# Kernel tuning notes

Hardware: AMD Instinct MI355X
Metric: run time of the kernel (lower is better)

The kernel has to match this reference:

```python
import jax, jax.numpy as jnp
import numpy as np


def setup_inputs() -> dict:
    key = jax.random.key(0)
    k1, k2, k3, k4 = jax.random.split(key, 4)
    N, E, F, H = 100000, 3200000, 128, 128
    x = jax.random.normal(k1, (N, F), dtype=jnp.float32)
    edge_index = jax.random.randint(k2, (2, E), 0, N, dtype=jnp.int64)
    # GCNConv learned params (glorot-like weight, zero-ish bias init replaced by small random)
    W = jax.random.normal(k3, (F, H), dtype=jnp.float32) * (1.0 / np.sqrt(F))
    b = jax.random.normal(k4, (H,), dtype=jnp.float32) * 0.01
    return {"x": x, "edge_index": edge_index, "W": W, "b": b}


def reference(x, edge_index, W, b):
    # PyG GCNConv: add self-loops, symmetric degree normalization,
    # linear transform, gather-scale-scatter aggregation, bias.
    N = x.shape[0]
    loop = jnp.arange(N, dtype=edge_index.dtype)
    src = jnp.concatenate([edge_index[0], loop])  # [E+N]
    dst = jnp.concatenate([edge_index[1], loop])  # [E+N]
    # degree of destination nodes (edge_weight = 1)
    deg = jax.ops.segment_sum(jnp.ones_like(dst, dtype=x.dtype), dst, num_segments=N)
    dinv = jnp.where(deg > 0, jax.lax.rsqrt(deg), 0.0)
    norm = dinv[src] * dinv[dst]  # [E+N]
    h = x @ W  # [N, H]
    msgs = norm[:, None] * h[src]  # gather + scale, [E+N, H]
    out = jax.ops.segment_sum(msgs, dst, num_segments=N)  # scatter-add
    return out + b
```

## Files before the change

kernel.cpp:

```cpp
#include <hip/hip_runtime.h>

#define FEAT 128
#define BSH 7
#define BNODES 128
#define ATILE 4096
#define MAXNB 1024
#define STILE 1024

typedef __attribute__((ext_vector_type(8))) short bf16x8;
typedef __attribute__((ext_vector_type(4))) float f32x4;

__global__ void k_zero_i32(int* __restrict__ p, int n) {
    int i = blockIdx.x * blockDim.x + threadIdx.x;
    if (i < n) p[i] = 0;
}

__global__ void k_count(const int* __restrict__ dst, int* __restrict__ cnt, int E) {
    int i = blockIdx.x * blockDim.x + threadIdx.x;
    if (i < E) atomicAdd(&cnt[dst[i]], 1);
}

__global__ void k_dinv(const int* __restrict__ cnt, float* __restrict__ dinv, int N) {
    int i = blockIdx.x * blockDim.x + threadIdx.x;
    if (i < N) dinv[i] = rsqrtf((float)cnt[i] + 1.0f);
}

__global__ void k_bucket_base(const int* __restrict__ offs, int* __restrict__ cur, int NB) {
    int b = blockIdx.x * blockDim.x + threadIdx.x;
    if (b < NB) cur[b] = offs[b << BSH];
}

__device__ inline unsigned int f2bf(float f) {
    unsigned int u = __float_as_uint(f);
    return (u + 0x7FFFu + ((u >> 16) & 1u)) >> 16;
}

__global__ void k_cvt_bf16(const float* __restrict__ x, unsigned int* __restrict__ xbf,
                           long long n8) {
    long long i = (long long)blockIdx.x * blockDim.x + threadIdx.x;
    if (i >= n8) return;
    float4 a = ((const float4*)x)[i * 2];
    float4 c = ((const float4*)x)[i * 2 + 1];
    uint4 o;
    o.x = f2bf(a.x) | (f2bf(a.y) << 16);
    o.y = f2bf(a.z) | (f2bf(a.w) << 16);
    o.z = f2bf(c.x) | (f2bf(c.y) << 16);
    o.w = f2bf(c.z) | (f2bf(c.w) << 16);
    ((uint4*)xbf)[i] = o;
}

__global__ void k_cvt_w(const float* __restrict__ W, unsigned short* __restrict__ wt) {
    int i = blockIdx.x * blockDim.x + threadIdx.x;
    if (i >= FEAT * FEAT) return;
    int n = i >> 7, k = i & 127;
    wt[i] = (unsigned short)f2bf(W[k * FEAT + n]);
}

__global__ __launch_bounds__(256) void k_hist_bucket(const int* __restrict__ dst,
                                                     int* __restrict__ bCnt, int E, int NB) {
    __shared__ int h[MAXNB];
    int tid = threadIdx.x;
    for (int i = tid; i < NB; i += 256) h[i] = 0;
    __syncthreads();
    int base = blockIdx.x * ATILE;
    int end = min(base + ATILE, E);
    for (int e = base + tid; e < end; e += 256)
        atomicAdd(&h[dst[e] >> BSH], 1);
    __syncthreads();
    for (int i = tid; i < NB; i += 256)
        if (h[i]) atomicAdd(&bCnt[i], h[i]);
}

__global__ void k_scan_bucket(const int* __restrict__ bCnt, int* __restrict__ bOffs,
                              int* __restrict__ cur, int NB, int E) {
    __shared__ int s[256];
    int t = threadIdx.x;
    int carry = 0;
    for (int base = 0; base < NB; base += 256) {
        int i = base + t;
        int v = (i < NB) ? bCnt[i] : 0;
        s[t] = v; __syncthreads();
        for (int o = 1; o < 256; o <<= 1) {
            int add = (t >= o) ? s[t - o] : 0;
            __syncthreads();
            s[t] += add;
            __syncthreads();
        }
        if (i < NB) { int ex = s[t] - v + carry; bOffs[i] = ex; cur[i] = ex; }
        __syncthreads();
        carry += s[255];
        __syncthreads();
    }
    if (t == 0) bOffs[NB] = E;
}

__global__ void k_scan_partial(const int* __restrict__ cnt, int* __restrict__ part, int N) {
    __shared__ int s[256];
    int base = blockIdx.x * STILE;
    int t = threadIdx.x;
    int sum = 0;
#pragma unroll
    for (int k = 0; k < 4; ++k) {
        int i = base + t * 4 + k;
        if (i < N) sum += cnt[i];
    }
    s[t] = sum; __syncthreads();
    for (int off = 128; off > 0; off >>= 1) {
        if (t < off) s[t] += s[t + off];
        __syncthreads();
    }
    if (t == 0) part[blockIdx.x] = s[0];
}

__global__ void k_scan_top(int* __restrict__ part, int nTiles) {
    __shared__ int s[256];
    int t = threadIdx.x;
    int carry = 0;
    for (int base = 0; base < nTiles; base += 256) {
        int i = base + t;
        int v = (i < nTiles) ? part[i] : 0;
        s[t] = v; __syncthreads();
        for (int o = 1; o < 256; o <<= 1) {
            int add = (t >= o) ? s[t - o] : 0;
            __syncthreads();
            s[t] += add;
            __syncthreads();
        }
        if (i < nTiles) part[i] = (s[t] - v) + carry;
        __syncthreads();
        carry += s[255];
        __syncthreads();
    }
}

__global__ void k_scan_final(const int* __restrict__ cnt, const int* __restrict__ part,
                             int* __restrict__ offs, int N) {
    __shared__ int s[256];
    int base = blockIdx.x * STILE;
    int t = threadIdx.x;
    int v[4]; int sum = 0;
#pragma unroll
    for (int k = 0; k < 4; ++k) {
        int i = base + t * 4 + k;
        v[k] = (i < N) ? cnt[i] : 0;
        sum += v[k];
    }
    s[t] = sum; __syncthreads();
    for (int o = 1; o < 256; o <<= 1) {
        int add = (t >= o) ? s[t - o] : 0;
        __syncthreads();
        s[t] += add;
        __syncthreads();
    }
    int excl = (s[t] - sum) + part[blockIdx.x];
#pragma unroll
    for (int k = 0; k < 4; ++k) {
        int i = base + t * 4 + k;
        if (i < N) offs[i] = excl;
        excl += v[k];
    }
}

__global__ __launch_bounds__(256) void k_bin(const int* __restrict__ src,
                                             const int* __restrict__ dst,
                                             int* __restrict__ cur,
                                             unsigned int* __restrict__ pairs,
                                             int E, int NB) {
    __shared__ int hist[MAXNB];
    __shared__ int tbase[MAXNB];
    __shared__ int sc[256];
    __shared__ unsigned int stM[ATILE];
    __shared__ unsigned short stB[ATILE];

    int tid = threadIdx.x;
    int tileBase = blockIdx.x * ATILE;
    int tileCnt = min(ATILE, E - tileBase);

    for (int i = tid; i < NB; i += 256) hist[i] = 0;
    __syncthreads();

    unsigned int pk[16]; unsigned short bk[16]; unsigned short rk[16];
#pragma unroll
    for (int k = 0; k < 16; ++k) {
        int e = tileBase + k * 256 + tid;
        if (e < E) {
            int s = src[e], d = dst[e];
            int b = d >> BSH;
            int r = atomicAdd(&hist[b], 1);
            pk[k] = (unsigned int)s | ((unsigned int)(d & (BNODES - 1)) << 24);
            bk[k] = (unsigned short)b;
            rk[k] = (unsigned short)r;
        }
    }
    __syncthreads();

    int per = (NB + 255) / 256;
    int myBase = tid * per;
    int partial = 0;
    for (int i = 0; i < per; ++i) {
        int idx = myBase + i;
        if (idx < NB) partial += hist[idx];
    }
    sc[tid] = partial;
    __syncthreads();
    for (int o = 1; o < 256; o <<= 1) {
        int add = (tid >= o) ? sc[tid - o] : 0;
        __syncthreads();
        sc[tid] += add;
        __syncthreads();
    }
    int run = (tid == 0) ? 0 : sc[tid - 1];
    for (int i = 0; i < per; ++i) {
        int idx = myBase + i;
        if (idx < NB) {
            int c = hist[idx];
            hist[idx] = run;
            if (c > 0) {
                int g = atomicAdd(&cur[idx], c);
                tbase[idx] = g - run;
            }
            run += c;
        }
    }
    __syncthreads();

#pragma unroll
    for (int k = 0; k < 16; ++k) {
        int e = tileBase + k * 256 + tid;
        if (e < E) {
            int slot = hist[bk[k]] + (int)rk[k];
            stM[slot] = pk[k];
            stB[slot] = bk[k];
        }
    }
    __syncthreads();

    for (int s = tid; s < tileCnt; s += 256) {
        int gpos = tbase[stB[s]] + s;
        pairs[gpos] = stM[s];
    }
}

__global__ __launch_bounds__(256) void k_fill_local2(const unsigned int* __restrict__ pairs,
                                                     const int* __restrict__ bOffs,
                                                     unsigned int* __restrict__ csr,
                                                     int* __restrict__ g_cnt,
                                                     int* __restrict__ g_offs,
                                                     float* __restrict__ g_dinv,
                                                     int N) {
    __shared__ int lcnt[BNODES];
    __shared__ int lexcl[BNODES];
    __shared__ int lcur[BNODES];
    int b = blockIdx.x;
    int node0 = b << BSH;
    int nn = min(BNODES, N - node0);
    int tid = threadIdx.x;
    int bstart = bOffs[b], bend = bOffs[b + 1];

    if (tid < BNODES) lcnt[tid] = 0;
    __syncthreads();
    for (int i = bstart + tid; i < bend; i += 256)
        atomicAdd(&lcnt[pairs[i] >> 24], 1);
    __syncthreads();
    if (tid < BNODES) lexcl[tid] = lcnt[tid];
    __syncthreads();
    for (int o = 1; o < BNODES; o <<= 1) {
        int add = (tid < BNODES && tid >= o) ? lexcl[tid - o] : 0;
        __syncthreads();
        if (tid < BNODES) lexcl[tid] += add;
        __syncthreads();
    }
    if (tid < BNODES) {
        int ex = bstart + lexcl[tid] - lcnt[tid];
        lcur[tid] = ex;
        if (tid < nn) {
            g_cnt[node0 + tid] = lcnt[tid];
            g_offs[node0 + tid] = ex;
            g_dinv[node0 + tid] = rsqrtf((float)lcnt[tid] + 1.0f);
        }
    }
    __syncthreads();
    for (int i = bstart + tid; i < bend; i += 256) {
        unsigned int p = pairs[i];
        int dl = (int)(p >> 24);
        int pos = atomicAdd(&lcur[dl], 1);
        csr[pos] = p & 0xFFFFFFu;
    }
}

__global__ __launch_bounds__(256) void k_fill_local(const unsigned int* __restrict__ pairs,
                                                    const int* __restrict__ offs,
                                                    unsigned int* __restrict__ csr,
                                                    int N, int E) {
    __shared__ int lcur[BNODES];
    int b = blockIdx.x;
    int node0 = b << BSH;
    int nn = min(BNODES, N - node0);
    int tid = threadIdx.x;
    for (int i = tid; i < nn; i += 256) lcur[i] = offs[node0 + i];
    __syncthreads();
    int start = offs[node0];
    int end = (node0 + BNODES >= N) ? E : offs[node0 + BNODES];
    for (int i = start + tid; i < end; i += 256) {
        unsigned int p = pairs[i];
        int dl = (int)(p >> 24);
        int pos = atomicAdd(&lcur[dl], 1);
        csr[pos] = p & 0xFFFFFFu;
    }
}

__global__ __launch_bounds__(256) void k_aggregate_bf2(const unsigned int* __restrict__ xbf,
                                                       const float* __restrict__ dinv,
                                                       const int* __restrict__ offs,
                                                       const int* __restrict__ cnt,
                                                       const unsigned int* __restrict__ csr,
                                                       unsigned int* __restrict__ aggbf,
                                                       int N) {
    int wid = (blockIdx.x * blockDim.x + threadIdx.x) >> 6;
    int lane = threadIdx.x & 63;
    if (wid >= N) return;
    int n = __builtin_amdgcn_readfirstlane(wid);

    float di = dinv[n];
    int start = offs[n];
    int m = cnt[n];

    unsigned int wself = xbf[(size_t)n * 64 + lane];
    float sl = di * di;
    float2 acc = make_float2(sl * __uint_as_float(wself << 16),
                             sl * __uint_as_float(wself & 0xFFFF0000u));

    int i = 0;
    for (; i + 8 <= m; i += 8) {
        int s[8]; float nr[8]; unsigned int w[8];
#pragma unroll
        for (int u = 0; u < 8; ++u) s[u] = (int)csr[start + i + u];
#pragma unroll
        for (int u = 0; u < 8; ++u) w[u] = xbf[(size_t)s[u] * 64 + lane];
#pragma unroll
        for (int u = 0; u < 8; ++u) nr[u] = dinv[s[u]] * di;
#pragma unroll
        for (int u = 0; u < 8; ++u) {
            acc.x += nr[u] * __uint_as_float(w[u] << 16);
            acc.y += nr[u] * __uint_as_float(w[u] & 0xFFFF0000u);
        }
    }
    for (; i + 4 <= m; i += 4) {
        int s0 = (int)csr[start + i];
        int s1 = (int)csr[start + i + 1];
        int s2 = (int)csr[start + i + 2];
        int s3 = (int)csr[start + i + 3];
        float n0 = dinv[s0] * di, n1 = dinv[s1] * di, n2 = dinv[s2] * di, n3 = dinv[s3] * di;
        unsigned int w0 = xbf[(size_t)s0 * 64 + lane];
        unsigned int w1 = xbf[(size_t)s1 * 64 + lane];
        unsigned int w2 = xbf[(size_t)s2 * 64 + lane];
        unsigned int w3 = xbf[(size_t)s3 * 64 + lane];
        acc.x += n0 * __uint_as_float(w0 << 16);
        acc.y += n0 * __uint_as_float(w0 & 0xFFFF0000u);
        acc.x += n1 * __uint_as_float(w1 << 16);
        acc.y += n1 * __uint_as_float(w1 & 0xFFFF0000u);
        acc.x += n2 * __uint_as_float(w2 << 16);
        acc.y += n2 * __uint_as_float(w2 & 0xFFFF0000u);
        acc.x += n3 * __uint_as_float(w3 << 16);
        acc.y += n3 * __uint_as_float(w3 & 0xFFFF0000u);
    }
    for (; i < m; ++i) {
        int s0 = (int)csr[start + i];
        float n0 = dinv[s0] * di;
        unsigned int w0 = xbf[(size_t)s0 * 64 + lane];
        acc.x += n0 * __uint_as_float(w0 << 16);
        acc.y += n0 * __uint_as_float(w0 & 0xFFFF0000u);
    }
    aggbf[(size_t)n * 64 + lane] = f2bf(acc.x) | (f2bf(acc.y) << 16);
}

__global__ __launch_bounds__(256) void k_aggregate_bf(const float* __restrict__ x,
                                                      const unsigned int* __restrict__ xbf,
                                                      const float* __restrict__ dinv,
                                                      const int* __restrict__ offs,
                                                      const int* __restrict__ cnt,
                                                      const unsigned int* __restrict__ csr,
                                                      float* __restrict__ out, int N) {
    int wid = (blockIdx.x * blockDim.x + threadIdx.x) >> 6;
    int lane = threadIdx.x & 63;
    if (wid >= N) return;
    int n = __builtin_amdgcn_readfirstlane(wid);

    float di = dinv[n];
    int start = offs[n];
    int m = cnt[n];

    float2 a = ((const float2*)(x + (size_t)n * FEAT))[lane];
    float sl = di * di;
    float2 acc = make_float2(a.x * sl, a.y * sl);

    int i = 0;
    for (; i + 4 <= m; i += 4) {
        int s0 = (int)csr[start + i];
        int s1 = (int)csr[start + i + 1];
        int s2 = (int)csr[start + i + 2];
        int s3 = (int)csr[start + i + 3];
        float n0 = dinv[s0] * di, n1 = dinv[s1] * di, n2 = dinv[s2] * di, n3 = dinv[s3] * di;
        unsigned int w0 = xbf[(size_t)s0 * 64 + lane];
        unsigned int w1 = xbf[(size_t)s1 * 64 + lane];
        unsigned int w2 = xbf[(size_t)s2 * 64 + lane];
        unsigned int w3 = xbf[(size_t)s3 * 64 + lane];
        acc.x += n0 * __uint_as_float(w0 << 16);
        acc.y += n0 * __uint_as_float(w0 & 0xFFFF0000u);
        acc.x += n1 * __uint_as_float(w1 << 16);
        acc.y += n1 * __uint_as_float(w1 & 0xFFFF0000u);
        acc.x += n2 * __uint_as_float(w2 << 16);
        acc.y += n2 * __uint_as_float(w2 & 0xFFFF0000u);
        acc.x += n3 * __uint_as_float(w3 << 16);
        acc.y += n3 * __uint_as_float(w3 & 0xFFFF0000u);
    }
    for (; i < m; ++i) {
        int s0 = (int)csr[start + i];
        float n0 = dinv[s0] * di;
        unsigned int w0 = xbf[(size_t)s0 * 64 + lane];
        acc.x += n0 * __uint_as_float(w0 << 16);
        acc.y += n0 * __uint_as_float(w0 & 0xFFFF0000u);
    }
    ((float2*)(out + (size_t)n * FEAT))[lane] = acc;
}

__global__ __launch_bounds__(256) void k_aggregate(const float* __restrict__ x,
                                                   const float* __restrict__ dinv,
                                                   const int* __restrict__ offs,
                                                   const int* __restrict__ cnt,
                                                   const unsigned int* __restrict__ csr,
                                                   float* __restrict__ out, int N) {
    int wid = (blockIdx.x * blockDim.x + threadIdx.x) >> 6;
    int lane = threadIdx.x & 63;
    if (wid >= N) return;
    int n = __builtin_amdgcn_readfirstlane(wid);

    float di = dinv[n];
    int start = offs[n];
    int m = cnt[n];

    float2 a = ((const float2*)(x + (size_t)n * FEAT))[lane];
    float sl = di * di;
    float2 acc = make_float2(a.x * sl, a.y * sl);

    int i = 0;
    for (; i + 4 <= m; i += 4) {
        int s0 = (int)csr[start + i];
        int s1 = (int)csr[start + i + 1];
        int s2 = (int)csr[start + i + 2];
        int s3 = (int)csr[start + i + 3];
        float n0 = dinv[s0] * di, n1 = dinv[s1] * di, n2 = dinv[s2] * di, n3 = dinv[s3] * di;
        float2 v0 = ((const float2*)(x + (size_t)s0 * FEAT))[lane];
        float2 v1 = ((const float2*)(x + (size_t)s1 * FEAT))[lane];
        float2 v2 = ((const float2*)(x + (size_t)s2 * FEAT))[lane];
        float2 v3 = ((const float2*)(x + (size_t)s3 * FEAT))[lane];
        acc.x += n0 * v0.x; acc.y += n0 * v0.y;
        acc.x += n1 * v1.x; acc.y += n1 * v1.y;
        acc.x += n2 * v2.x; acc.y += n2 * v2.y;
        acc.x += n3 * v3.x; acc.y += n3 * v3.y;
    }
    for (; i < m; ++i) {
        int s0 = (int)csr[start + i];
        float n0 = dinv[s0] * di;
        float2 v0 = ((const float2*)(x + (size_t)s0 * FEAT))[lane];
        acc.x += n0 * v0.x; acc.y += n0 * v0.y;
    }
    ((float2*)(out + (size_t)n * FEAT))[lane] = acc;
}

__global__ __launch_bounds__(256) void k_gemm_mfma2(const unsigned short* __restrict__ abf,
                                                    const unsigned short* __restrict__ wt,
                                                    const float* __restrict__ bias,
                                                    float* __restrict__ out, int N) {
    int tid = threadIdx.x;
    int wave = tid >> 6, l = tid & 63;
    int lm = l & 15, lg = l >> 4;
    int rowA = blockIdx.x * 128 + wave * 32;

    f32x4 acc[2][8];
#pragma unroll
    for (int mt = 0; mt < 2; ++mt)
#pragma unroll
        for (int nt = 0; nt < 8; ++nt)
            acc[mt][nt] = (f32x4){0.f, 0.f, 0.f, 0.f};

#pragma unroll
    for (int kk = 0; kk < 4; ++kk) {
        int k = kk * 32 + lg * 8;
        bf16x8 afr[2];
#pragma unroll
        for (int mt = 0; mt < 2; ++mt) {
            int r = rowA + mt * 16 + lm;
            if (r < N)
                afr[mt] = *(const bf16x8*)(abf + (size_t)r * FEAT + k);
            else
                afr[mt] = (bf16x8){0, 0, 0, 0, 0, 0, 0, 0};
        }
#pragma unroll
        for (int nt = 0; nt < 8; ++nt) {
            int col = nt * 16 + lm;
            bf16x8 bfr = *(const bf16x8*)(wt + (size_t)col * FEAT + k);
            acc[0][nt] = __builtin_amdgcn_mfma_f32_16x16x32_bf16(afr[0], bfr, acc[0][nt], 0, 0, 0);
            acc[1][nt] = __builtin_amdgcn_mfma_f32_16x16x32_bf16(afr[1], bfr, acc[1][nt], 0, 0, 0);
        }
    }

#pragma unroll
    for (int nt = 0; nt < 8; ++nt) {
        int col = nt * 16 + lm;
        float bv = bias[col];
#pragma unroll
        for (int mt = 0; mt < 2; ++mt) {
#pragma unroll
            for (int r = 0; r < 4; ++r) {
                int row = rowA + mt * 16 + lg * 4 + r;
                if (row < N) out[(size_t)row * FEAT + col] = acc[mt][nt][r] + bv;
            }
        }
    }
}

__global__ __launch_bounds__(256) void k_gemm_mfma(float* __restrict__ out,
                                                   const unsigned short* __restrict__ wt,
                                                   const float* __restrict__ b, int N) {
    int tid = threadIdx.x;
    int wave = tid >> 6, l = tid & 63;
    int lm = l & 15, lg = l >> 4;
    int rowA = blockIdx.x * 128 + wave * 32;

    f32x4 acc[2][8];
#pragma unroll
    for (int mt = 0; mt < 2; ++mt)
#pragma unroll
        for (int nt = 0; nt < 8; ++nt)
            acc[mt][nt] = (f32x4){0.f, 0.f, 0.f, 0.f};

#pragma unroll
    for (int kk = 0; kk < 4; ++kk) {
        int k = kk * 32 + lg * 8;
        bf16x8 afr[2];
#pragma unroll
        for (int mt = 0; mt < 2; ++mt) {
            int r = rowA + mt * 16 + lm;
            float4 f0 = make_float4(0.f, 0.f, 0.f, 0.f);
            float4 f1 = make_float4(0.f, 0.f, 0.f, 0.f);
            if (r < N) {
                const float* p = out + (size_t)r * FEAT + k;
                f0 = *(const float4*)p;
                f1 = *(const float4*)(p + 4);
            }
            afr[mt][0] = (short)f2bf(f0.x);
            afr[mt][1] = (short)f2bf(f0.y);
            afr[mt][2] = (short)f2bf(f0.z);
            afr[mt][3] = (short)f2bf(f0.w);
            afr[mt][4] = (short)f2bf(f1.x);
            afr[mt][5] = (short)f2bf(f1.y);
            afr[mt][6] = (short)f2bf(f1.z);
            afr[mt][7] = (short)f2bf(f1.w);
        }
#pragma unroll
        for (int nt = 0; nt < 8; ++nt) {
            int col = nt * 16 + lm;
            bf16x8 bfr = *(const bf16x8*)(wt + (size_t)col * FEAT + k);
            acc[0][nt] = __builtin_amdgcn_mfma_f32_16x16x32_bf16(afr[0], bfr, acc[0][nt], 0, 0, 0);
            acc[1][nt] = __builtin_amdgcn_mfma_f32_16x16x32_bf16(afr[1], bfr, acc[1][nt], 0, 0, 0);
        }
    }

#pragma unroll
    for (int nt = 0; nt < 8; ++nt) {
        int col = nt * 16 + lm;
        float bv = b[col];
#pragma unroll
        for (int mt = 0; mt < 2; ++mt) {
#pragma unroll
            for (int r = 0; r < 4; ++r) {
                int row = rowA + mt * 16 + lg * 4 + r;
                if (row < N) out[(size_t)row * FEAT + col] = acc[mt][nt][r] + bv;
            }
        }
    }
}

__global__ __launch_bounds__(256) void k_gemm_inplace(float* __restrict__ out,
                                                      const float* __restrict__ W,
                                                      const float* __restrict__ b, int N) {
    __shared__ float Wl[FEAT * FEAT];
    int tid = threadIdx.x;
    for (int i = tid; i < FEAT * FEAT / 4; i += 256)
        ((float4*)Wl)[i] = ((const float4*)W)[i];
    __syncthreads();

    int j = tid & 127;
    int half = tid >> 7;
    int row0 = blockIdx.x * 16 + half * 8;
    row0 = __builtin_amdgcn_readfirstlane(row0);

    float bj = b[j];
    float acc[8];
#pragma unroll
    for (int r = 0; r < 8; ++r) acc[r] = bj;

    const float* Y = out + (size_t)row0 * FEAT;
    bool full = (row0 + 8 <= N);
    if (full) {
        for (int f4 = 0; f4 < FEAT; f4 += 4) {
            float w0 = Wl[(f4 + 0) * FEAT + j];
            float w1 = Wl[(f4 + 1) * FEAT + j];
            float w2 = Wl[(f4 + 2) * FEAT + j];
            float w3 = Wl[(f4 + 3) * FEAT + j];
#pragma unroll
            for (int r = 0; r < 8; ++r) {
                float4 y = *(const float4*)&Y[(size_t)r * FEAT + f4];
                acc[r] += w0 * y.x + w1 * y.y + w2 * y.z + w3 * y.w;
            }
        }
    } else {
        for (int f = 0; f < FEAT; ++f) {
            float w = Wl[f * FEAT + j];
            for (int r = 0; r < 8; ++r)
                if (row0 + r < N) acc[r] += w * Y[(size_t)r * FEAT + f];
        }
    }
    __syncthreads();
    if (full) {
#pragma unroll
        for (int r = 0; r < 8; ++r) out[(size_t)(row0 + r) * FEAT + j] = acc[r];
    } else {
        for (int r = 0; r < 8; ++r)
            if (row0 + r < N) out[(size_t)(row0 + r) * FEAT + j] = acc[r];
    }
}

__global__ void k_fill_direct(const int* __restrict__ src, const int* __restrict__ dst,
                              int* __restrict__ cur, unsigned int* __restrict__ csr, int E) {
    int e = blockIdx.x * blockDim.x + threadIdx.x;
    if (e < E) {
        int d = dst[e];
        int p = atomicAdd(&cur[d], 1);
        csr[p] = (unsigned int)src[e];
    }
}
__global__ void k_copy_i32(const int* __restrict__ a, int* __restrict__ b, int n) {
    int i = blockIdx.x * blockDim.x + threadIdx.x;
    if (i < n) b[i] = a[i];
}
__global__ void k_deg_initf(float* __restrict__ deg, int N) {
    int i = blockIdx.x * blockDim.x + threadIdx.x;
    if (i < N) deg[i] = 1.0f;
}
__global__ void k_deg_countf(const int* __restrict__ dst, float* __restrict__ deg, int E) {
    int i = blockIdx.x * blockDim.x + threadIdx.x;
    if (i < E) atomicAdd(&deg[dst[i]], 1.0f);
}
__global__ void k_rsqrtf_(float* __restrict__ deg, int N) {
    int i = blockIdx.x * blockDim.x + threadIdx.x;
    if (i < N) deg[i] = rsqrtf(deg[i]);
}
__global__ void k_selfloop(const float* __restrict__ x, const float* __restrict__ dinv,
                           float* __restrict__ out, int N) {
    int t = blockIdx.x * blockDim.x + threadIdx.x;
    int n = t >> 5, c = t & 31;
    if (n >= N) return;
    float s = dinv[n]; s *= s;
    float4 v = ((const float4*)(x + (size_t)n * FEAT))[c];
    v.x *= s; v.y *= s; v.z *= s; v.w *= s;
    ((float4*)(out + (size_t)n * FEAT))[c] = v;
}
__global__ void k_scatter(const int* __restrict__ src, const int* __restrict__ dst,
                          const float* __restrict__ dinv, const float* __restrict__ x,
                          float* __restrict__ out, int E) {
    long long gid = (long long)blockIdx.x * blockDim.x + threadIdx.x;
    long long e = gid >> 6;
    int lane = threadIdx.x & 63;
    if (e >= E) return;
    int s = src[e], d = dst[e];
    float nrm = dinv[s] * dinv[d];
    const float* xs = x + (size_t)s * FEAT;
    float* od = out + (size_t)d * FEAT;
    atomicAdd(&od[lane],      nrm * xs[lane]);
    atomicAdd(&od[lane + 64], nrm * xs[lane + 64]);
}

extern "C" void kernel_launch(void* const* d_in, const int* in_sizes, int n_in,
                              void* d_out, int out_size, void* d_ws, size_t ws_size,
                              hipStream_t stream) {
    const float* x = (const float*)d_in[0];
    const int*   ei = (const int*)d_in[1];
    const float* W = (const float*)d_in[2];
    const float* b = (const float*)d_in[3];
    float* out = (float*)d_out;

    int N = in_sizes[0] / FEAT;
    int E = in_sizes[1] / 2;
    const int* src = ei;
    const int* dst = ei + E;

    const int bs = 256;
    int nTiles = (N + STILE - 1) / STILE;
    int NB = (N + BNODES - 1) >> BSH;
    int binGrid = (E + ATILE - 1) / ATILE;

    size_t off = 0;
    auto take = [&](size_t bytes) {
        size_t r = off;
        off = (off + bytes + 255) & ~(size_t)255;
        return r;
    };
    size_t o_dinv  = take(4 * (size_t)N);
    size_t o_cnt   = take(4 * (size_t)N);
    size_t o_offs  = take(4 * (size_t)N);
    size_t o_bcnt  = take(4 * (size_t)NB);
    size_t o_boffs = take(4 * (size_t)(NB + 1));
    size_t o_cur   = take(4 * (size_t)NB);
    size_t o_pairs = take(4 * (size_t)E);
    size_t o_csr   = take(4 * (size_t)E);
    size_t o_xbf   = take(4 * (size_t)N * 64);
    size_t o_wbf   = take(2 * (size_t)FEAT * FEAT);
    size_t need_preA = off;
    size_t o_aggbf = take(4 * (size_t)N * 64);
    size_t need_A = off;

    bool okNB = (NB <= MAXNB) && (N <= (1 << 24));
    bool can_A = okNB && (ws_size >= need_A);

    if (can_A) {
        char* base = (char*)d_ws;
        float* dinv = (float*)(base + o_dinv);
        int* cnt  = (int*)(base + o_cnt);
        int* offs = (int*)(base + o_offs);
        int* bCnt = (int*)(base + o_bcnt);
        int* bOffs= (int*)(base + o_boffs);
        int* cur  = (int*)(base + o_cur);
        unsigned int* pairs = (unsigned int*)(base + o_pairs);
        unsigned int* csr   = (unsigned int*)(base + o_csr);
        unsigned int* xbf   = (unsigned int*)(base + o_xbf);
        unsigned short* wbf = (unsigned short*)(base + o_wbf);
        unsigned int* aggbf = (unsigned int*)(base + o_aggbf);

        k_zero_i32<<<(NB + bs - 1) / bs, bs, 0, stream>>>(bCnt, NB);
        k_hist_bucket<<<binGrid, 256, 0, stream>>>(dst, bCnt, E, NB);
        k_scan_bucket<<<1, 256, 0, stream>>>(bCnt, bOffs, cur, NB, E);
        k_bin<<<binGrid, 256, 0, stream>>>(src, dst, cur, pairs, E, NB);
        k_fill_local2<<<NB, 256, 0, stream>>>(pairs, bOffs, csr, cnt, offs, dinv, N);

        long long n8 = (long long)N * (FEAT / 8);
        k_cvt_bf16<<<(int)((n8 + bs - 1) / bs), bs, 0, stream>>>(x, xbf, n8);
        k_cvt_w<<<(FEAT * FEAT + bs - 1) / bs, bs, 0, stream>>>(W, wbf);

        long long t_ag = (long long)N * 64;
        k_aggregate_bf2<<<(int)((t_ag + bs - 1) / bs), bs, 0, stream>>>(
            xbf, dinv, offs, cnt, csr, aggbf, N);
        k_gemm_mfma2<<<(N + 127) / 128, 256, 0, stream>>>(
            (const unsigned short*)aggbf, wbf, b, out, N);
        return;
    }

    size_t need_direct = (4 * (size_t)N + nTiles + (size_t)E) * 4;
    size_t need_bin    = (4 * (size_t)N + nTiles + 2 * (size_t)E) * 4;
    size_t need_bf     = need_bin + (size_t)N * 64 * 4 + (size_t)FEAT * FEAT * 2;

    float* dinv = (float*)d_ws;
    int* cnt  = (int*)d_ws + N;
    int* offs = (int*)d_ws + 2 * (size_t)N;
    int* cur  = (int*)d_ws + 3 * (size_t)N;
    int* part = (int*)d_ws + 4 * (size_t)N;
    unsigned int* pairs = (unsigned int*)(part + nTiles);
    unsigned int* csr_bin = pairs + E;
    unsigned int* xbf = csr_bin + E;
    unsigned short* wbf = (unsigned short*)(xbf + (size_t)N * 64);
    unsigned int* csr_dir = pairs;

    bool can_bin    = (ws_size >= need_bin) && okNB;
    bool can_bf     = can_bin && (ws_size >= need_bf);
    bool can_direct = (ws_size >= need_direct);

    if (can_bin || can_direct) {
        k_zero_i32<<<(N + bs - 1) / bs, bs, 0, stream>>>(cnt, N);
        k_count<<<(E + bs - 1) / bs, bs, 0, stream>>>(dst, cnt, E);
        k_dinv<<<(N + bs - 1) / bs, bs, 0, stream>>>(cnt, dinv, N);
        k_scan_partial<<<nTiles, 256, 0, stream>>>(cnt, part, N);
        k_scan_top<<<1, 256, 0, stream>>>(part, nTiles);
        k_scan_final<<<nTiles, 256, 0, stream>>>(cnt, part, offs, N);

        unsigned int* csr;
        if (can_bin) {
            csr = csr_bin;
            k_bucket_base<<<(NB + bs - 1) / bs, bs, 0, stream>>>(offs, cur, NB);
            k_bin<<<binGrid, 256, 0, stream>>>(src, dst, cur, pairs, E, NB);
            k_fill_local<<<NB, 256, 0, stream>>>(pairs, offs, csr, N, E);
        } else {
            csr = csr_dir;
            k_copy_i32<<<(N + bs - 1) / bs, bs, 0, stream>>>(offs, cur, N);
            k_fill_direct<<<(E + bs - 1) / bs, bs, 0, stream>>>(src, dst, cur, csr, E);
        }

        long long t_ag = (long long)N * 64;
        if (can_bf) {
            long long n8 = (long long)N * (FEAT / 8);
            k_cvt_bf16<<<(int)((n8 + bs - 1) / bs), bs, 0, stream>>>(x, xbf, n8);
            k_cvt_w<<<(FEAT * FEAT + bs - 1) / bs, bs, 0, stream>>>(W, wbf);
            k_aggregate_bf<<<(int)((t_ag + bs - 1) / bs), bs, 0, stream>>>(
                x, xbf, dinv, offs, cnt, csr, out, N);
            k_gemm_mfma<<<(N + 127) / 128, 256, 0, stream>>>(out, wbf, b, N);
        } else {
            k_aggregate<<<(int)((t_ag + bs - 1) / bs), bs, 0, stream>>>(
                x, dinv, offs, cnt, csr, out, N);
            k_gemm_inplace<<<(N + 15) / 16, 256, 0, stream>>>(out, W, b, N);
        }
    } else {
        float* deg = (float*)d_ws;
        k_deg_initf<<<(N + bs - 1) / bs, bs, 0, stream>>>(deg, N);
        k_deg_countf<<<(E + bs - 1) / bs, bs, 0, stream>>>(dst, deg, E);
        k_rsqrtf_<<<(N + bs - 1) / bs, bs, 0, stream>>>(deg, N);
        long long t_sl = (long long)N * 32;
        k_selfloop<<<(int)((t_sl + bs - 1) / bs), bs, 0, stream>>>(x, deg, out, N);
        long long t_sc = (long long)E * 64;
        k_scatter<<<(int)((t_sc + bs - 1) / bs), bs, 0, stream>>>(src, dst, deg, x, out, E);
        k_gemm_inplace<<<(N + 15) / 16, 256, 0, stream>>>(out, W, b, N);
    }
}
```

Baseline: 291.0 us.

## Fuse aggregation with MFMA GEMM and merge preprocessing kernels

Replaces the separate bf16 aggregation and GEMM kernels with one kernel. Each wave aggregates 16 nodes into LDS as bf16 rows, then runs the 128x128 MFMA transform and writes output with bias. This removes the global round trip of the aggregated matrix. The zeroing, x conversion and W conversion launches are also merged into a single kernel to cut launch overhead. The trade-off is that each wave now processes 16 nodes one after another, which lowers the memory-level parallelism of the gather and can cause load imbalance from degree variance.

```diff
diff --git a/kernel.cpp b/kernel.cpp
--- a/kernel.cpp
+++ b/kernel.cpp
@@ -33,6 +33,42 @@
 __device__ inline unsigned int f2bf(float f) {
     unsigned int u = __float_as_uint(f);
     return (u + 0x7FFFu + ((u >> 16) & 1u)) >> 16;
+}
+
+__global__ __launch_bounds__(256) void k_pre(const float* __restrict__ x,
+                                             unsigned int* __restrict__ xbf,
+                                             const float* __restrict__ W,
+                                             unsigned short* __restrict__ wt,
+                                             int* __restrict__ bCnt,
+                                             long long n8, int NB,
+                                             int zb, int cb, int wb) {
+    int blk = blockIdx.x;
+    if (blk < zb) {
+        int i = blk * 256 + threadIdx.x;
+        if (i < NB) bCnt[i] = 0;
+        return;
+    }
+    blk -= zb;
+    if (blk < cb) {
+        long long i = (long long)blk * 256 + threadIdx.x;
+        if (i >= n8) return;
+        float4 a = ((const float4*)x)[i * 2];
+        float4 c = ((const float4*)x)[i * 2 + 1];
+        uint4 o;
+        o.x = f2bf(a.x) | (f2bf(a.y) << 16);
+        o.y = f2bf(a.z) | (f2bf(a.w) << 16);
+        o.z = f2bf(c.x) | (f2bf(c.y) << 16);
+        o.w = f2bf(c.z) | (f2bf(c.w) << 16);
+        ((uint4*)xbf)[i] = o;
+        return;
+    }
+    blk -= cb;
+    if (blk < wb) {
+        int i = blk * 256 + threadIdx.x;
+        if (i >= FEAT * FEAT) return;
+        int n = i >> 7, k = i & 127;
+        wt[i] = (unsigned short)f2bf(W[k * FEAT + n]);
+    }
 }
 
 __global__ void k_cvt_bf16(const float* __restrict__ x, unsigned int* __restrict__ xbf,
@@ -48,7 +84,6 @@
     o.w = f2bf(c.z) | (f2bf(c.w) << 16);
     ((uint4*)xbf)[i] = o;
 }
-
 __global__ void k_cvt_w(const float* __restrict__ W, unsigned short* __restrict__ wt) {
     int i = blockIdx.x * blockDim.x + threadIdx.x;
     if (i >= FEAT * FEAT) return;
@@ -288,24 +323,86 @@
     }
 }
 
-__global__ __launch_bounds__(256) void k_fill_local(const unsigned int* __restrict__ pairs,
-                                                    const int* __restrict__ offs,
-                                                    unsigned int* __restrict__ csr,
-                                                    int N, int E) {
-    __shared__ int lcur[BNODES];
-    int b = blockIdx.x;
-    int node0 = b << BSH;
-    int nn = min(BNODES, N - node0);
+#define RSTRIDE 68
+__global__ __launch_bounds__(512) void k_agg_gemm(const unsigned int* __restrict__ xbf,
+                                                  const float* __restrict__ dinv,
+                                                  const int* __restrict__ offs,
+                                                  const int* __restrict__ cnt,
+                                                  const unsigned int* __restrict__ csr,
+                                                  const unsigned short* __restrict__ wt,
+                                                  const float* __restrict__ bias,
+                                                  float* __restrict__ out, int N) {
+    __shared__ unsigned int rows[8 * 16 * RSTRIDE];
     int tid = threadIdx.x;
-    for (int i = tid; i < nn; i += 256) lcur[i] = offs[node0 + i];
-    __syncthreads();
-    int start = offs[node0];
-    int end = (node0 + BNODES >= N) ? E : offs[node0 + BNODES];
-    for (int i = start + tid; i < end; i += 256) {
-        unsigned int p = pairs[i];
-        int dl = (int)(p >> 24);
-        int pos = atomicAdd(&lcur[dl], 1);
-        csr[pos] = p & 0xFFFFFFu;
+    int wave = tid >> 6, lane = tid & 63;
+    int nodeBase = (blockIdx.x << BSH) + wave * 16;
+    unsigned int* my = rows + wave * 16 * RSTRIDE;
+
+    if (nodeBase < N) {
+        int nlim = min(16, N - nodeBase);
+        for (int i = 0; i < nlim; ++i) {
+            int n = nodeBase + i;
+            float di = dinv[n];
+            int start = offs[n];
+            int m = cnt[n];
+
+            unsigned int wself = xbf[(size_t)n * 64 + lane];
+            float sl = di * di;
+            float2 acc = make_float2(sl * __uint_as_float(wself << 16),
+                                     sl * __uint_as_float(wself & 0xFFFF0000u));
+
+            int e = 0;
+            for (; e + 8 <= m; e += 8) {
+                int s[8]; float nr[8]; unsigned int w[8];
+#pragma unroll
+                for (int u = 0; u < 8; ++u) s[u] = (int)csr[start + e + u];
+#pragma unroll
+                for (int u = 0; u < 8; ++u) w[u] = xbf[(size_t)s[u] * 64 + lane];
+#pragma unroll
+                for (int u = 0; u < 8; ++u) nr[u] = dinv[s[u]] * di;
+#pragma unroll
+                for (int u = 0; u < 8; ++u) {
+                    acc.x += nr[u] * __uint_as_float(w[u] << 16);
+                    acc.y += nr[u] * __uint_as_float(w[u] & 0xFFFF0000u);
+                }
+            }
+            for (; e < m; ++e) {
+                int s0 = (int)csr[start + e];
+                float n0 = dinv[s0] * di;
+                unsigned int w0 = xbf[(size_t)s0 * 64 + lane];
+                acc.x += n0 * __uint_as_float(w0 << 16);
+                acc.y += n0 * __uint_as_float(w0 & 0xFFFF0000u);
+            }
+            my[i * RSTRIDE + lane] = f2bf(acc.x) | (f2bf(acc.y) << 16);
+        }
+
+        int lm = lane & 15, lg = lane >> 4;
+        f32x4 acc[8];
+#pragma unroll
+        for (int nt = 0; nt < 8; ++nt) acc[nt] = (f32x4){0.f, 0.f, 0.f, 0.f};
+
+#pragma unroll
+        for (int kk = 0; kk < 4; ++kk) {
+            int k = kk * 32 + lg * 8;
+            bf16x8 afr = *(const bf16x8*)((const unsigned short*)(my + lm * RSTRIDE) + k);
+#pragma unroll
+            for (int nt = 0; nt < 8; ++nt) {
+                int col = nt * 16 + lm;
+                bf16x8 bfr = *(const bf16x8*)(wt + (size_t)col * FEAT + k);
+                acc[nt] = __builtin_amdgcn_mfma_f32_16x16x32_bf16(afr, bfr, acc[nt], 0, 0, 0);
+            }
+        }
+
+#pragma unroll
+        for (int nt = 0; nt < 8; ++nt) {
+            int col = nt * 16 + lm;
+            float bv = bias[col];
+#pragma unroll
+            for (int r = 0; r < 4; ++r) {
+                int row = nodeBase + lg * 4 + r;
+                if (row < N) out[(size_t)row * FEAT + col] = acc[nt][r] + bv;
+            }
+        }
     }
 }
 
@@ -345,25 +442,6 @@
             acc.y += nr[u] * __uint_as_float(w[u] & 0xFFFF0000u);
         }
     }
-    for (; i + 4 <= m; i += 4) {
-        int s0 = (int)csr[start + i];
-        int s1 = (int)csr[start + i + 1];
-        int s2 = (int)csr[start + i + 2];
-        int s3 = (int)csr[start + i + 3];
-        float n0 = dinv[s0] * di, n1 = dinv[s1] * di, n2 = dinv[s2] * di, n3 = dinv[s3] * di;
-        unsigned int w0 = xbf[(size_t)s0 * 64 + lane];
-        unsigned int w1 = xbf[(size_t)s1 * 64 + lane];
-        unsigned int w2 = xbf[(size_t)s2 * 64 + lane];
-        unsigned int w3 = xbf[(size_t)s3 * 64 + lane];
-        acc.x += n0 * __uint_as_float(w0 << 16);
-        acc.y += n0 * __uint_as_float(w0 & 0xFFFF0000u);
-        acc.x += n1 * __uint_as_float(w1 << 16);
-        acc.y += n1 * __uint_as_float(w1 & 0xFFFF0000u);
-        acc.x += n2 * __uint_as_float(w2 << 16);
-        acc.y += n2 * __uint_as_float(w2 & 0xFFFF0000u);
-        acc.x += n3 * __uint_as_float(w3 << 16);
-        acc.y += n3 * __uint_as_float(w3 & 0xFFFF0000u);
-    }
     for (; i < m; ++i) {
         int s0 = (int)csr[start + i];
         float n0 = dinv[s0] * di;
@@ -374,54 +452,77 @@
     aggbf[(size_t)n * 64 + lane] = f2bf(acc.x) | (f2bf(acc.y) << 16);
 }
 
-__global__ __launch_bounds__(256) void k_aggregate_bf(const float* __restrict__ x,
-                                                      const unsigned int* __restrict__ xbf,
-                                                      const float* __restrict__ dinv,
-                                                      const int* __restrict__ offs,
-                                                      const int* __restrict__ cnt,
-                                                      const unsigned int* __restrict__ csr,
-                                                      float* __restrict__ out, int N) {
-    int wid = (blockIdx.x * blockDim.x + threadIdx.x) >> 6;
-    int lane = threadIdx.x & 63;
-    if (wid >= N) return;
-    int n = __builtin_amdgcn_readfirstlane(wid);
-
-    float di = dinv[n];
-    int start = offs[n];
-    int m = cnt[n];
-
-    float2 a = ((const float2*)(x + (size_t)n * FEAT))[lane];
-    float sl = di * di;
-    float2 acc = make_float2(a.x * sl, a.y * sl);
-
-    int i = 0;
-    for (; i + 4 <= m; i += 4) {
-        int s0 = (int)csr[start + i];
-        int s1 = (int)csr[start + i + 1];
-        int s2 = (int)csr[start + i + 2];
-        int s3 = (int)csr[start + i + 3];
-        float n0 = dinv[s0] * di, n1 = dinv[s1] * di, n2 = dinv[s2] * di, n3 = dinv[s3] * di;
-        unsigned int w0 = xbf[(size_t)s0 * 64 + lane];
-        unsigned int w1 = xbf[(size_t)s1 * 64 + lane];
-        unsigned int w2 = xbf[(size_t)s2 * 64 + lane];
-        unsigned int w3 = xbf[(size_t)s3 * 64 + lane];
-        acc.x += n0 * __uint_as_float(w0 << 16);
-        acc.y += n0 * __uint_as_float(w0 & 0xFFFF0000u);
-        acc.x += n1 * __uint_as_float(w1 << 16);
-        acc.y += n1 * __uint_as_float(w1 & 0xFFFF0000u);
-        acc.x += n2 * __uint_as_float(w2 << 16);
-        acc.y += n2 * __uint_as_float(w2 & 0xFFFF0000u);
-        acc.x += n3 * __uint_as_float(w3 << 16);
-        acc.y += n3 * __uint_as_float(w3 & 0xFFFF0000u);
-    }
-    for (; i < m; ++i) {
-        int s0 = (int)csr[start + i];
-        float n0 = dinv[s0] * di;
-        unsigned int w0 = xbf[(size_t)s0 * 64 + lane];
-        acc.x += n0 * __uint_as_float(w0 << 16);
-        acc.y += n0 * __uint_as_float(w0 & 0xFFFF0000u);
-    }
-    ((float2*)(out + (size_t)n * FEAT))[lane] = acc;
+__global__ __launch_bounds__(256) void k_gemm_mfma2(const unsigned short* __restrict__ abf,
+                                                    const unsigned short* __restrict__ wt,
+                                                    const float* __restrict__ bias,
+                                                    float* __restrict__ out, int N) {
+    int tid = threadIdx.x;
+    int wave = tid >> 6, l = tid & 63;
+    int lm = l & 15, lg = l >> 4;
+    int rowA = blockIdx.x * 128 + wave * 32;
+
+    f32x4 acc[2][8];
+#pragma unroll
+    for (int mt = 0; mt < 2; ++mt)
+#pragma unroll
+        for (int nt = 0; nt < 8; ++nt)
+            acc[mt][nt] = (f32x4){0.f, 0.f, 0.f, 0.f};
+
+#pragma unroll
+    for (int kk = 0; kk < 4; ++kk) {
+        int k = kk * 32 + lg * 8;
+        bf16x8 afr[2];
+#pragma unroll
+        for (int mt = 0; mt < 2; ++mt) {
+            int r = rowA + mt * 16 + lm;
+            if (r < N)
+                afr[mt] = *(const bf16x8*)(abf + (size_t)r * FEAT + k);
+            else
+                afr[mt] = (bf16x8){0, 0, 0, 0, 0, 0, 0, 0};
+        }
+#pragma unroll
+        for (int nt = 0; nt < 8; ++nt) {
+            int col = nt * 16 + lm;
+            bf16x8 bfr = *(const bf16x8*)(wt + (size_t)col * FEAT + k);
+            acc[0][nt] = __builtin_amdgcn_mfma_f32_16x16x32_bf16(afr[0], bfr, acc[0][nt], 0, 0, 0);
+            acc[1][nt] = __builtin_amdgcn_mfma_f32_16x16x32_bf16(afr[1], bfr, acc[1][nt], 0, 0, 0);
+        }
+    }
+
+#pragma unroll
+    for (int nt = 0; nt < 8; ++nt) {
+        int col = nt * 16 + lm;
+        float bv = bias[col];
+#pragma unroll
+        for (int mt = 0; mt < 2; ++mt) {
+#pragma unroll
+            for (int r = 0; r < 4; ++r) {
+                int row = rowA + mt * 16 + lg * 4 + r;
+                if (row < N) out[(size_t)row * FEAT + col] = acc[mt][nt][r] + bv;
+            }
+        }
+    }
+}
+
+__global__ __launch_bounds__(256) void k_fill_local(const unsigned int* __restrict__ pairs,
+                                                    const int* __restrict__ offs,
+                                                    unsigned int* __restrict__ csr,
+                                                    int N, int E) {
+    __shared__ int lcur[BNODES];
+    int b = blockIdx.x;
+    int node0 = b << BSH;
+    int nn = min(BNODES, N - node0);
+    int tid = threadIdx.x;
+    for (int i = tid; i < nn; i += 256) lcur[i] = offs[node0 + i];
+    __syncthreads();
+    int start = offs[node0];
+    int end = (node0 + BNODES >= N) ? E : offs[node0 + BNODES];
+    for (int i = start + tid; i < end; i += 256) {
+        unsigned int p = pairs[i];
+        int dl = (int)(p >> 24);
+        int pos = atomicAdd(&lcur[dl], 1);
+        csr[pos] = p & 0xFFFFFFu;
+    }
 }
 
 __global__ __launch_bounds__(256) void k_aggregate(const float* __restrict__ x,
@@ -466,120 +567,6 @@
         acc.x += n0 * v0.x; acc.y += n0 * v0.y;
     }
     ((float2*)(out + (size_t)n * FEAT))[lane] = acc;
-}
-
-__global__ __launch_bounds__(256) void k_gemm_mfma2(const unsigned short* __restrict__ abf,
-                                                    const unsigned short* __restrict__ wt,
-                                                    const float* __restrict__ bias,
-                                                    float* __restrict__ out, int N) {
-    int tid = threadIdx.x;
-    int wave = tid >> 6, l = tid & 63;
-    int lm = l & 15, lg = l >> 4;
-    int rowA = blockIdx.x * 128 + wave * 32;
-
-    f32x4 acc[2][8];
-#pragma unroll
-    for (int mt = 0; mt < 2; ++mt)
-#pragma unroll
-        for (int nt = 0; nt < 8; ++nt)
-            acc[mt][nt] = (f32x4){0.f, 0.f, 0.f, 0.f};
-
-#pragma unroll
-    for (int kk = 0; kk < 4; ++kk) {
-        int k = kk * 32 + lg * 8;
-        bf16x8 afr[2];
-#pragma unroll
-        for (int mt = 0; mt < 2; ++mt) {
-            int r = rowA + mt * 16 + lm;
-            if (r < N)
-                afr[mt] = *(const bf16x8*)(abf + (size_t)r * FEAT + k);
-            else
-                afr[mt] = (bf16x8){0, 0, 0, 0, 0, 0, 0, 0};
-        }
-#pragma unroll
-        for (int nt = 0; nt < 8; ++nt) {
-            int col = nt * 16 + lm;
-            bf16x8 bfr = *(const bf16x8*)(wt + (size_t)col * FEAT + k);
-            acc[0][nt] = __builtin_amdgcn_mfma_f32_16x16x32_bf16(afr[0], bfr, acc[0][nt], 0, 0, 0);
-            acc[1][nt] = __builtin_amdgcn_mfma_f32_16x16x32_bf16(afr[1], bfr, acc[1][nt], 0, 0, 0);
-        }
-    }
-
-#pragma unroll
-    for (int nt = 0; nt < 8; ++nt) {
-        int col = nt * 16 + lm;
-        float bv = bias[col];
-#pragma unroll
-        for (int mt = 0; mt < 2; ++mt) {
-#pragma unroll
-            for (int r = 0; r < 4; ++r) {
-                int row = rowA + mt * 16 + lg * 4 + r;
-                if (row < N) out[(size_t)row * FEAT + col] = acc[mt][nt][r] + bv;
-            }
-        }
-    }
-}
-
-__global__ __launch_bounds__(256) void k_gemm_mfma(float* __restrict__ out,
-                                                   const unsigned short* __restrict__ wt,
-                                                   const float* __restrict__ b, int N) {
-    int tid = threadIdx.x;
-    int wave = tid >> 6, l = tid & 63;
-    int lm = l & 15, lg = l >> 4;
-    int rowA = blockIdx.x * 128 + wave * 32;
-
-    f32x4 acc[2][8];
-#pragma unroll
-    for (int mt = 0; mt < 2; ++mt)
-#pragma unroll
-        for (int nt = 0; nt < 8; ++nt)
-            acc[mt][nt] = (f32x4){0.f, 0.f, 0.f, 0.f};
-
-#pragma unroll
-    for (int kk = 0; kk < 4; ++kk) {
-        int k = kk * 32 + lg * 8;
-        bf16x8 afr[2];
-#pragma unroll
-        for (int mt = 0; mt < 2; ++mt) {
-            int r = rowA + mt * 16 + lm;
-            float4 f0 = make_float4(0.f, 0.f, 0.f, 0.f);
-            float4 f1 = make_float4(0.f, 0.f, 0.f, 0.f);
-            if (r < N) {
-                const float* p = out + (size_t)r * FEAT + k;
-                f0 = *(const float4*)p;
-                f1 = *(const float4*)(p + 4);
-            }
-            afr[mt][0] = (short)f2bf(f0.x);
-            afr[mt][1] = (short)f2bf(f0.y);
-            afr[mt][2] = (short)f2bf(f0.z);
-            afr[mt][3] = (short)f2bf(f0.w);
-            afr[mt][4] = (short)f2bf(f1.x);
-            afr[mt][5] = (short)f2bf(f1.y);
-            afr[mt][6] = (short)f2bf(f1.z);
-            afr[mt][7] = (short)f2bf(f1.w);
-        }
-#pragma unroll
-        for (int nt = 0; nt < 8; ++nt) {
-            int col = nt * 16 + lm;
-            bf16x8 bfr = *(const bf16x8*)(wt + (size_t)col * FEAT + k);
-            acc[0][nt] = __builtin_amdgcn_mfma_f32_16x16x32_bf16(afr[0], bfr, acc[0][nt], 0, 0, 0);
-            acc[1][nt] = __builtin_amdgcn_mfma_f32_16x16x32_bf16(afr[1], bfr, acc[1][nt], 0, 0, 0);
-        }
-    }
-
-#pragma unroll
-    for (int nt = 0; nt < 8; ++nt) {
-        int col = nt * 16 + lm;
-        float bv = b[col];
-#pragma unroll
-        for (int mt = 0; mt < 2; ++mt) {
-#pragma unroll
-            for (int r = 0; r < 4; ++r) {
-                int row = rowA + mt * 16 + lg * 4 + r;
-                if (row < N) out[(size_t)row * FEAT + col] = acc[mt][nt][r] + bv;
-            }
-        }
-    }
 }
 
 __global__ __launch_bounds__(256) void k_gemm_inplace(float* __restrict__ out,
@@ -717,8 +704,6 @@
     size_t o_csr   = take(4 * (size_t)E);
     size_t o_xbf   = take(4 * (size_t)N * 64);
     size_t o_wbf   = take(2 * (size_t)FEAT * FEAT);
-    size_t need_preA = off;
-    size_t o_aggbf = take(4 * (size_t)N * 64);
     size_t need_A = off;
 
     bool okNB = (NB <= MAXNB) && (N <= (1 << 24));
@@ -736,29 +721,25 @@
         unsigned int* csr   = (unsigned int*)(base + o_csr);
         unsigned int* xbf   = (unsigned int*)(base + o_xbf);
         unsigned short* wbf = (unsigned short*)(base + o_wbf);
-        unsigned int* aggbf = (unsigned int*)(base + o_aggbf);
-
-        k_zero_i32<<<(NB + bs - 1) / bs, bs, 0, stream>>>(bCnt, NB);
+
+        long long n8 = (long long)N * (FEAT / 8);
+        int zb = (NB + 255) / 256;
+        int cb = (int)((n8 + 255) / 256);
+        int wb = (FEAT * FEAT + 255) / 256;
+
+        k_pre<<<zb + cb + wb, 256, 0, stream>>>(x, xbf, W, wbf, bCnt, n8, NB, zb, cb, wb);
         k_hist_bucket<<<binGrid, 256, 0, stream>>>(dst, bCnt, E, NB);
         k_scan_bucket<<<1, 256, 0, stream>>>(bCnt, bOffs, cur, NB, E);
         k_bin<<<binGrid, 256, 0, stream>>>(src, dst, cur, pairs, E, NB);
         k_fill_local2<<<NB, 256, 0, stream>>>(pairs, bOffs, csr, cnt, offs, dinv, N);
-
-        long long n8 = (long long)N * (FEAT / 8);
-        k_cvt_bf16<<<(int)((n8 + bs - 1) / bs), bs, 0, stream>>>(x, xbf, n8);
-        k_cvt_w<<<(FEAT * FEAT + bs - 1) / bs, bs, 0, stream>>>(W, wbf);
-
-        long long t_ag = (long long)N * 64;
-        k_aggregate_bf2<<<(int)((t_ag + bs - 1) / bs), bs, 0, stream>>>(
-            xbf, dinv, offs, cnt, csr, aggbf, N);
-        k_gemm_mfma2<<<(N + 127) / 128, 256, 0, stream>>>(
-            (const unsigned short*)aggbf, wbf, b, out, N);
+        k_agg_gemm<<<NB, 512, 0, stream>>>(xbf, dinv, offs, cnt, csr, wbf, b, out, N);
         return;
     }
 
     size_t need_direct = (4 * (size_t)N + nTiles + (size_t)E) * 4;
     size_t need_bin    = (4 * (size_t)N + nTiles + 2 * (size_t)E) * 4;
-    size_t need_bf     = need_bin + (size_t)N * 64 * 4 + (size_t)FEAT * FEAT * 2;
+    size_t need_bf     = need_bin + (size_t)N * 64 * 4 + (size_t)FEAT * FEAT * 2 +
+                         (size_t)N * 64 * 4;
 
     float* dinv = (float*)d_ws;
     int* cnt  = (int*)d_ws + N;
@@ -769,6 +750,7 @@
     unsigned int* csr_bin = pairs + E;
     unsigned int* xbf = csr_bin + E;
     unsigned short* wbf = (unsigned short*)(xbf + (size_t)N * 64);
+    unsigned int* aggbf = (unsigned int*)(wbf + (size_t)FEAT * FEAT);
     unsigned int* csr_dir = pairs;
 
     bool can_bin    = (ws_size >= need_bin) && okNB;
@@ -800,9 +782,10 @@
             long long n8 = (long long)N * (FEAT / 8);
             k_cvt_bf16<<<(int)((n8 + bs - 1) / bs), bs, 0, stream>>>(x, xbf, n8);
             k_cvt_w<<<(FEAT * FEAT + bs - 1) / bs, bs, 0, stream>>>(W, wbf);
-            k_aggregate_bf<<<(int)((t_ag + bs - 1) / bs), bs, 0, stream>>>(
-                x, xbf, dinv, offs, cnt, csr, out, N);
-            k_gemm_mfma<<<(N + 127) / 128, 256, 0, stream>>>(out, wbf, b, N);
+            k_aggregate_bf2<<<(int)((t_ag + bs - 1) / bs), bs, 0, stream>>>(
+                xbf, dinv, offs, cnt, csr, aggbf, N);
+            k_gemm_mfma2<<<(N + 127) / 128, 256, 0, stream>>>(
+                (const unsigned short*)aggbf, wbf, b, out, N);
         } else {
             k_aggregate<<<(int)((t_ag + bs - 1) / bs), bs, 0, stream>>>(
                 x, dinv, offs, cnt, csr, out, N);
```

After: 353.5 us. 21.5% more time.
